# Kernel tuning notes

Measured on AMD Instinct MI355X. Metric: run time of the kernel, lower is better.

The kernel has to match this reference:

```python
import jax, jax.numpy as jnp
import numpy as np

B, S, Q, C = 1, 128, 256, 256
H, DH = 8, 32
TOT = H * DH  # 256


def setup_inputs() -> dict:
    key = jax.random.key(0)
    ks = jax.random.split(key, 12)
    inp = {
        'q_x': jax.random.normal(ks[0], (B, S, Q, C), jnp.float32),
        'kv_x': jax.random.normal(ks[1], (B, S, Q, C), jnp.float32),
        'bias_mask': jax.random.normal(ks[2], (B, S, 1, 1, Q), jnp.float32),
        'bias_pair': jax.random.normal(ks[3], (B, 1, H, Q, Q), jnp.float32),
        # torch nn.Linear weights are (out_features, in_features)
        'Wq': jax.random.normal(ks[4], (TOT, C), jnp.float32) * (C ** -0.5),
        'Wk': jax.random.normal(ks[5], (TOT, C), jnp.float32) * (C ** -0.5),
        'Wv': jax.random.normal(ks[6], (TOT, C), jnp.float32) * (C ** -0.5),
        'Wg': jax.random.normal(ks[7], (TOT, C), jnp.float32) * 0.02,
        'bg': jnp.ones((TOT,), jnp.float32),   # 'gating' init: zero W, bias=1
        'Wo': jax.random.normal(ks[8], (C, TOT), jnp.float32) * 0.02,
        'bo': jnp.zeros((C,), jnp.float32),
    }
    return inp


def reference(q_x, kv_x, bias_mask, bias_pair, Wq, Wk, Wv, Wg, bg, Wo, bo):
    # QKV projections (no bias), split heads, move head dim before Q: [B,S,H,Q,DH]
    def proj(x, W):
        y = jnp.einsum('bsqc,dc->bsqd', x, W)
        return y.reshape(*y.shape[:-1], H, DH).transpose(0, 1, 3, 2, 4)

    q = proj(q_x, Wq)   # NOTE: literal source applies NO 1/sqrt(dh) scaling in naive mode
    k = proj(kv_x, Wk)
    v = proj(kv_x, Wv)

    # scores [B,S,H,Q,K] with additive biases, manual softmax
    scores = jnp.einsum('bshqd,bshkd->bshqk', q, k) + bias_mask + bias_pair
    a = jax.nn.softmax(scores, axis=-1)
    o = jnp.einsum('bshqk,bshkd->bshqd', a, v)
    o = o.transpose(0, 1, 3, 2, 4)  # [B,S,Q,H,DH]

    # gating
    g = jax.nn.sigmoid(jnp.einsum('bsqc,dc->bsqd', q_x, Wg) + bg)
    o = o * g.reshape(*g.shape[:-1], H, DH)

    # output projection
    o = o.reshape(*o.shape[:-2], TOT)
    return jnp.einsum('bsqd,cd->bsqc', o, Wo) + bo
```

## Files before the change

### kernel.cpp

```cpp
#include <hip/hip_runtime.h>


typedef unsigned short u16;
typedef unsigned int   u32;
typedef float  f32x4  __attribute__((ext_vector_type(4)));
typedef __bf16 bf16x8 __attribute__((ext_vector_type(8)));

__device__ __forceinline__ float bf2f(u16 u) {
    union { u32 i; float f; } v; v.i = ((u32)u) << 16; return v.f;
}
__device__ __forceinline__ u16 f2bf(float f) {
    __bf16 h = (__bf16)f; return __builtin_bit_cast(u16, h);
}

__device__ __forceinline__ void gld16(const u16* g, u16* l) {
    __builtin_amdgcn_global_load_lds(
        (const __attribute__((address_space(1))) u32*)g,
        (__attribute__((address_space(3))) u32*)l, 16, 0, 0);
}

__device__ __forceinline__ void cvt8(const float4* src, u16* dst) {
    float4 a = src[0], b = src[1];
    u16 r[8];
    r[0] = f2bf(a.x); r[1] = f2bf(a.y); r[2] = f2bf(a.z); r[3] = f2bf(a.w);
    r[4] = f2bf(b.x); r[5] = f2bf(b.y); r[6] = f2bf(b.z); r[7] = f2bf(b.w);
    *(uint4*)dst = *(uint4*)r;
}

__global__ __launch_bounds__(256) void prep(
    const float* __restrict__ qx, const float* __restrict__ kvx,
    const float* __restrict__ Wq, const float* __restrict__ Wk,
    const float* __restrict__ Wv, const float* __restrict__ Wg,
    const float* __restrict__ Wo,
    u16* __restrict__ Xq, u16* __restrict__ Xkv, u16* __restrict__ Wball)
{
    const int b = blockIdx.x, t = threadIdx.x;
    if (b < 4096) {
        const int e = (b * 256 + t) * 8;
        cvt8((const float4*)(qx + e), Xq + e);
    } else if (b < 8192) {
        const int e = ((b - 4096) * 256 + t) * 8;
        cvt8((const float4*)(kvx + e), Xkv + e);
    } else {
        const int b2  = b - 8192;
        const int mat = b2 >> 5;
        const float* W = (mat == 0) ? Wq : (mat == 1) ? Wk : (mat == 2) ? Wv
                       : (mat == 3) ? Wg : Wo;
        const int off = (b2 & 31) * 2048 + t * 8;
        cvt8((const float4*)(W + off), Wball + mat * 65536 + off);
    }
}

__global__ __launch_bounds__(256) void proj_all(
    const u16* __restrict__ Xq, const u16* __restrict__ Xkv,
    const u16* __restrict__ Wball, const float* __restrict__ bg,
    u16* __restrict__ Qb, u16* __restrict__ Kb, u16* __restrict__ Vb, u16* __restrict__ Gb)
{
    __shared__ u16 At[128 * 64];
    __shared__ u16 Wt[128 * 64];

    const int bid = blockIdx.x;
    const int mb  = bid & 255;
    const int nb  = bid >> 8;
    const int t   = nb >> 1;
    const int n0  = (nb & 1) * 128;
    const int m0  = mb * 128;
    const u16* A = (t == 0 || t == 3) ? Xq : Xkv;
    const u16* W = Wball + t * 65536;
    u16*       O = (t == 0) ? Qb : (t == 1) ? Kb : (t == 2) ? Vb : Gb;

    const int tid  = threadIdx.x;
    const int lane = tid & 63;
    const int w    = tid >> 6;
    const int quad = lane >> 4;
    const int ln   = lane & 15;
    const int wm   = (w >> 1) * 64;
    const int wn   = (w & 1) * 64;
    const int lrow = lane >> 3;
    const int lcol = (lane & 7) * 8;

    f32x4 acc[4][4] = {};

    for (int k0 = 0; k0 < 256; k0 += 64) {
        __syncthreads();
        #pragma unroll
        for (int qq = 0; qq < 4; ++qq) {
            const int r = w * 32 + qq * 8;
            gld16(A + (size_t)(m0 + r + lrow) * 256 + k0 + lcol, &At[r * 64]);
            gld16(W + (size_t)(n0 + r + lrow) * 256 + k0 + lcol, &Wt[r * 64]);
        }
        __syncthreads();

        #pragma unroll
        for (int kk = 0; kk < 2; ++kk) {
            const int kc = kk * 32 + quad * 8;
            bf16x8 af[4], bfr[4];
            #pragma unroll
            for (int i = 0; i < 4; ++i)
                af[i] = __builtin_bit_cast(bf16x8, *(const uint4*)&At[(wm + i * 16 + ln) * 64 + kc]);
            #pragma unroll
            for (int j = 0; j < 4; ++j)
                bfr[j] = __builtin_bit_cast(bf16x8, *(const uint4*)&Wt[(wn + j * 16 + ln) * 64 + kc]);
            #pragma unroll
            for (int i = 0; i < 4; ++i)
                #pragma unroll
                for (int j = 0; j < 4; ++j)
                    acc[i][j] = __builtin_amdgcn_mfma_f32_16x16x32_bf16(af[i], bfr[j], acc[i][j], 0, 0, 0);
        }
    }

    const int act = (t == 3);
    #pragma unroll
    for (int i = 0; i < 4; ++i) {
        #pragma unroll
        for (int j = 0; j < 4; ++j) {
            #pragma unroll
            for (int rr = 0; rr < 4; ++rr) {
                const int row = m0 + wm + i * 16 + quad * 4 + rr;
                const int col = n0 + wn + j * 16 + ln;
                float v = acc[i][j][rr];
                if (act) { v += bg[col]; v = 1.0f / (1.0f + __expf(-v)); }
                O[(size_t)row * 256 + col] = f2bf(v);
            }
        }
    }
}

__global__ __launch_bounds__(256) void gemm_out(
    const u16* __restrict__ Ob, const u16* __restrict__ Wob,
    const float* __restrict__ bo, float* __restrict__ out)
{
    __shared__ u16 At[64 * 64];
    __shared__ u16 Wt[128 * 64];

    const int bid = blockIdx.x;
    const int m0  = (bid & 511) * 64;
    const int n0  = (bid >> 9) * 128;

    const int tid  = threadIdx.x;
    const int lane = tid & 63;
    const int w    = tid >> 6;
    const int quad = lane >> 4;
    const int ln   = lane & 15;
    const int wm   = (w >> 1) * 32;
    const int wn   = (w & 1) * 64;
    const int lrow = lane >> 3;
    const int lcol = (lane & 7) * 8;

    f32x4 acc[2][4] = {};

    for (int k0 = 0; k0 < 256; k0 += 64) {
        __syncthreads();
        #pragma unroll
        for (int qq = 0; qq < 2; ++qq) {
            const int r = w * 16 + qq * 8;
            gld16(Ob + (size_t)(m0 + r + lrow) * 256 + k0 + lcol, &At[r * 64]);
        }
        #pragma unroll
        for (int qq = 0; qq < 4; ++qq) {
            const int r = w * 32 + qq * 8;
            gld16(Wob + (size_t)(n0 + r + lrow) * 256 + k0 + lcol, &Wt[r * 64]);
        }
        __syncthreads();

        #pragma unroll
        for (int kk = 0; kk < 2; ++kk) {
            const int kc = kk * 32 + quad * 8;
            bf16x8 af[2], bfr[4];
            #pragma unroll
            for (int i = 0; i < 2; ++i)
                af[i] = __builtin_bit_cast(bf16x8, *(const uint4*)&At[(wm + i * 16 + ln) * 64 + kc]);
            #pragma unroll
            for (int j = 0; j < 4; ++j)
                bfr[j] = __builtin_bit_cast(bf16x8, *(const uint4*)&Wt[(wn + j * 16 + ln) * 64 + kc]);
            #pragma unroll
            for (int i = 0; i < 2; ++i)
                #pragma unroll
                for (int j = 0; j < 4; ++j)
                    acc[i][j] = __builtin_amdgcn_mfma_f32_16x16x32_bf16(af[i], bfr[j], acc[i][j], 0, 0, 0);
        }
    }

    #pragma unroll
    for (int i = 0; i < 2; ++i) {
        #pragma unroll
        for (int j = 0; j < 4; ++j) {
            #pragma unroll
            for (int rr = 0; rr < 4; ++rr) {
                const int row = m0 + wm + i * 16 + quad * 4 + rr;
                const int col = n0 + wn + j * 16 + ln;
                out[(size_t)row * 256 + col] = acc[i][j][rr] + bo[col];
            }
        }
    }
}

__global__ __launch_bounds__(256) void attn_kernel(
    const u16* __restrict__ Qb, const u16* __restrict__ Kb, const u16* __restrict__ Vb,
    const u16* __restrict__ Gb, const float* __restrict__ bm, const float* __restrict__ bp,
    u16* __restrict__ Ob)
{
    __shared__ u16   Vt[32][264];
    __shared__ u16   Pl[4][16][268];
    __shared__ float bmf[256];

    const int hs   = blockIdx.x;
    const int h    = hs & 7;
    const int s    = hs >> 3;
    const int qt   = blockIdx.y;
    const int tid  = threadIdx.x;
    const int lane = tid & 63;
    const int w    = tid >> 6;
    const int quad = lane >> 4;
    const int ln   = lane & 15;

    {
        const uint4* vp = (const uint4*)(Vb + (size_t)(s * 256 + tid) * 256 + h * 32);
        uint4 vv0 = vp[0], vv1 = vp[1], vv2 = vp[2], vv3 = vp[3];
        u16 tmp[32];
        *(uint4*)&tmp[0]  = vv0; *(uint4*)&tmp[8]  = vv1;
        *(uint4*)&tmp[16] = vv2; *(uint4*)&tmp[24] = vv3;
        #pragma unroll
        for (int dh = 0; dh < 32; ++dh) Vt[dh][tid] = tmp[dh];
        bmf[tid] = bm[s * 256 + tid];
    }
    __syncthreads();

    const int q0 = qt * 64 + w * 16;

    bf16x8 aq = __builtin_bit_cast(bf16x8,
        *(const uint4*)(Qb + (size_t)(s * 256 + q0 + ln) * 256 + h * 32 + quad * 8));

    f32x4 sc[16];
    #pragma unroll
    for (int nt = 0; nt < 16; ++nt) {
        bf16x8 bk = __builtin_bit_cast(bf16x8,
            *(const uint4*)(Kb + (size_t)(s * 256 + nt * 16 + ln) * 256 + h * 32 + quad * 8));
        f32x4 z = {0.f, 0.f, 0.f, 0.f};
        sc[nt] = __builtin_amdgcn_mfma_f32_16x16x32_bf16(aq, bk, z, 0, 0, 0);
    }

    float rmax[4] = {-1e30f, -1e30f, -1e30f, -1e30f};
    #pragma unroll
    for (int nt = 0; nt < 16; ++nt) {
        const int kp = nt * 16 + ln;
        const float bmv = bmf[kp];
        #pragma unroll
        for (int rr = 0; rr < 4; ++rr) {
            const int q = q0 + quad * 4 + rr;
            float v = sc[nt][rr] + bmv + bp[(size_t)(h * 256 + q) * 256 + kp];
            sc[nt][rr] = v;
            rmax[rr] = fmaxf(rmax[rr], v);
        }
    }
    #pragma unroll
    for (int rr = 0; rr < 4; ++rr) {
        float m = rmax[rr];
        m = fmaxf(m, __shfl_xor(m, 1));
        m = fmaxf(m, __shfl_xor(m, 2));
        m = fmaxf(m, __shfl_xor(m, 4));
        m = fmaxf(m, __shfl_xor(m, 8));
        rmax[rr] = m;
    }
    float rsum[4] = {0.f, 0.f, 0.f, 0.f};
    #pragma unroll
    for (int nt = 0; nt < 16; ++nt)
        #pragma unroll
        for (int rr = 0; rr < 4; ++rr) {
            float p = __expf(sc[nt][rr] - rmax[rr]);
            sc[nt][rr] = p;
            rsum[rr] += p;
        }
    float rinv[4];
    #pragma unroll
    for (int rr = 0; rr < 4; ++rr) {
        float t = rsum[rr];
        t += __shfl_xor(t, 1);
        t += __shfl_xor(t, 2);
        t += __shfl_xor(t, 4);
        t += __shfl_xor(t, 8);
        rinv[rr] = 1.0f / t;
    }

    #pragma unroll
    for (int nt = 0; nt < 16; ++nt)
        #pragma unroll
        for (int rr = 0; rr < 4; ++rr)
            Pl[w][quad * 4 + rr][nt * 16 + ln] = f2bf(sc[nt][rr] * rinv[rr]);

    f32x4 o0 = {0.f, 0.f, 0.f, 0.f}, o1 = {0.f, 0.f, 0.f, 0.f};
    #pragma unroll
    for (int kc = 0; kc < 8; ++kc) {
        bf16x8 pa = __builtin_bit_cast(bf16x8, *(const uint4*)&Pl[w][ln][kc * 32 + quad * 8]);
        bf16x8 v0 = __builtin_bit_cast(bf16x8, *(const uint4*)&Vt[ln][kc * 32 + quad * 8]);
        bf16x8 v1 = __builtin_bit_cast(bf16x8, *(const uint4*)&Vt[16 + ln][kc * 32 + quad * 8]);
        o0 = __builtin_amdgcn_mfma_f32_16x16x32_bf16(pa, v0, o0, 0, 0, 0);
        o1 = __builtin_amdgcn_mfma_f32_16x16x32_bf16(pa, v1, o1, 0, 0, 0);
    }

    #pragma unroll
    for (int rr = 0; rr < 4; ++rr) {
        const int q = q0 + quad * 4 + rr;
        const size_t base = (size_t)(s * 256 + q) * 256 + h * 32;
        float g0 = bf2f(Gb[base + ln]);
        float g1 = bf2f(Gb[base + 16 + ln]);
        Ob[base + ln]      = f2bf(o0[rr] * g0);
        Ob[base + 16 + ln] = f2bf(o1[rr] * g1);
    }
}

extern "C" void kernel_launch(void* const* d_in, const int* in_sizes, int n_in,
                              void* d_out, int out_size, void* d_ws, size_t ws_size,
                              hipStream_t stream)
{
    const float* qx  = (const float*)d_in[0];
    const float* kvx = (const float*)d_in[1];
    const float* bm  = (const float*)d_in[2];
    const float* bp  = (const float*)d_in[3];
    const float* Wq  = (const float*)d_in[4];
    const float* Wk  = (const float*)d_in[5];
    const float* Wv  = (const float*)d_in[6];
    const float* Wg  = (const float*)d_in[7];
    const float* bg  = (const float*)d_in[8];
    const float* Wo  = (const float*)d_in[9];
    const float* bo  = (const float*)d_in[10];
    float* out = (float*)d_out;

    const size_t NEL = (size_t)32768 * 256;
    u16* Qb = (u16*)d_ws;
    u16* Kb = Qb + NEL;
    u16* Vb = Kb + NEL;
    u16* Gb = Vb + NEL;
    u16* Wball = Gb + NEL;

    u16* Xq  = (u16*)d_out;
    u16* Xkv = Xq + NEL;

    prep<<<dim3(8352), dim3(256), 0, stream>>>(qx, kvx, Wq, Wk, Wv, Wg, Wo, Xq, Xkv, Wball);

    proj_all<<<dim3(2048), dim3(256), 0, stream>>>(Xq, Xkv, Wball, bg, Qb, Kb, Vb, Gb);

    attn_kernel<<<dim3(1024, 4), dim3(256), 0, stream>>>(Qb, Kb, Vb, Gb, bm, bp, Qb );

    gemm_out<<<dim3(1024), dim3(256), 0, stream>>>(Qb , Wball + 4 * 65536, bo, out);
}
```

Before: 250.1 us.

## Store Q/K/V/G projections in head-major layout for contiguous attention loads

Projection outputs now go to a [H][S][Q][DH] head-major layout instead of row-major [S*Q][256], and the attention and output GEMM kernels index through the new mapping. Each attention block's Q, K, V and G reads become one contiguous 16 KB region per (head, s) rather than 64-byte pieces strided by 512 bytes, which should improve coalescing and cache-line use. The cost is scattered 2-byte stores in the projection epilogue across head slabs, and gemm_out's A-tile loads now gather from four head slabs per 64-column k-chunk.

```diff
diff --git a/kernel.cpp b/kernel.cpp
--- a/kernel.cpp
+++ b/kernel.cpp
@@ -17,6 +17,11 @@
     __builtin_amdgcn_global_load_lds(
         (const __attribute__((address_space(1))) u32*)g,
         (__attribute__((address_space(3))) u32*)l, 16, 0, 0);
+}
+
+__device__ __forceinline__ size_t hm(int row, int col) {
+    const int s = row >> 8, q = row & 255, h = col >> 5, dh = col & 31;
+    return ((size_t)((h * 128 + s) * 256 + q) << 5) + dh;
 }
 
 __device__ __forceinline__ void cvt8(const float4* src, u16* dst) {
@@ -54,7 +59,7 @@
 __global__ __launch_bounds__(256) void proj_all(
     const u16* __restrict__ Xq, const u16* __restrict__ Xkv,
     const u16* __restrict__ Wball, const float* __restrict__ bg,
-    u16* __restrict__ Qb, u16* __restrict__ Kb, u16* __restrict__ Vb, u16* __restrict__ Gb)
+    u16* __restrict__ Qh, u16* __restrict__ Kh, u16* __restrict__ Vh, u16* __restrict__ Gh)
 {
     __shared__ u16 At[128 * 64];
     __shared__ u16 Wt[128 * 64];
@@ -67,7 +72,7 @@
     const int m0  = mb * 128;
     const u16* A = (t == 0 || t == 3) ? Xq : Xkv;
     const u16* W = Wball + t * 65536;
-    u16*       O = (t == 0) ? Qb : (t == 1) ? Kb : (t == 2) ? Vb : Gb;
+    u16*       O = (t == 0) ? Qh : (t == 1) ? Kh : (t == 2) ? Vh : Gh;
 
     const int tid  = threadIdx.x;
     const int lane = tid & 63;
@@ -120,14 +125,14 @@
                 const int col = n0 + wn + j * 16 + ln;
                 float v = acc[i][j][rr];
                 if (act) { v += bg[col]; v = 1.0f / (1.0f + __expf(-v)); }
-                O[(size_t)row * 256 + col] = f2bf(v);
+                O[hm(row, col)] = f2bf(v);
             }
         }
     }
 }
 
 __global__ __launch_bounds__(256) void gemm_out(
-    const u16* __restrict__ Ob, const u16* __restrict__ Wob,
+    const u16* __restrict__ Oh, const u16* __restrict__ Wob,
     const float* __restrict__ bo, float* __restrict__ out)
 {
     __shared__ u16 At[64 * 64];
@@ -154,7 +159,7 @@
         #pragma unroll
         for (int qq = 0; qq < 2; ++qq) {
             const int r = w * 16 + qq * 8;
-            gld16(Ob + (size_t)(m0 + r + lrow) * 256 + k0 + lcol, &At[r * 64]);
+            gld16(Oh + hm(m0 + r + lrow, k0 + lcol), &At[r * 64]);
         }
         #pragma unroll
         for (int qq = 0; qq < 4; ++qq) {
@@ -196,9 +201,9 @@
 }
 
 __global__ __launch_bounds__(256) void attn_kernel(
-    const u16* __restrict__ Qb, const u16* __restrict__ Kb, const u16* __restrict__ Vb,
-    const u16* __restrict__ Gb, const float* __restrict__ bm, const float* __restrict__ bp,
-    u16* __restrict__ Ob)
+    const u16* __restrict__ Qh, const u16* __restrict__ Kh, const u16* __restrict__ Vh,
+    const u16* __restrict__ Gh, const float* __restrict__ bm, const float* __restrict__ bp,
+    u16* __restrict__ Oh)
 {
     __shared__ u16   Vt[32][264];
     __shared__ u16   Pl[4][16][268];
@@ -214,8 +219,10 @@
     const int quad = lane >> 4;
     const int ln   = lane & 15;
 
+    const size_t hsBase = ((size_t)(h * 128 + s) * 256) << 5;
+
     {
-        const uint4* vp = (const uint4*)(Vb + (size_t)(s * 256 + tid) * 256 + h * 32);
+        const uint4* vp = (const uint4*)(Vh + hsBase + (size_t)tid * 32);
         uint4 vv0 = vp[0], vv1 = vp[1], vv2 = vp[2], vv3 = vp[3];
         u16 tmp[32];
         *(uint4*)&tmp[0]  = vv0; *(uint4*)&tmp[8]  = vv1;
@@ -229,13 +236,13 @@
     const int q0 = qt * 64 + w * 16;
 
     bf16x8 aq = __builtin_bit_cast(bf16x8,
-        *(const uint4*)(Qb + (size_t)(s * 256 + q0 + ln) * 256 + h * 32 + quad * 8));
+        *(const uint4*)(Qh + hsBase + (size_t)(q0 + ln) * 32 + quad * 8));
 
     f32x4 sc[16];
     #pragma unroll
     for (int nt = 0; nt < 16; ++nt) {
         bf16x8 bk = __builtin_bit_cast(bf16x8,
-            *(const uint4*)(Kb + (size_t)(s * 256 + nt * 16 + ln) * 256 + h * 32 + quad * 8));
+            *(const uint4*)(Kh + hsBase + (size_t)(nt * 16 + ln) * 32 + quad * 8));
         f32x4 z = {0.f, 0.f, 0.f, 0.f};
         sc[nt] = __builtin_amdgcn_mfma_f32_16x16x32_bf16(aq, bk, z, 0, 0, 0);
     }
@@ -301,11 +308,11 @@
     #pragma unroll
     for (int rr = 0; rr < 4; ++rr) {
         const int q = q0 + quad * 4 + rr;
-        const size_t base = (size_t)(s * 256 + q) * 256 + h * 32;
-        float g0 = bf2f(Gb[base + ln]);
-        float g1 = bf2f(Gb[base + 16 + ln]);
-        Ob[base + ln]      = f2bf(o0[rr] * g0);
-        Ob[base + 16 + ln] = f2bf(o1[rr] * g1);
+        const size_t base = hsBase + (size_t)q * 32;
+        float g0 = bf2f(Gh[base + ln]);
+        float g1 = bf2f(Gh[base + 16 + ln]);
+        Oh[base + ln]      = f2bf(o0[rr] * g0);
+        Oh[base + 16 + ln] = f2bf(o1[rr] * g1);
     }
 }
 
@@ -327,20 +334,20 @@
     float* out = (float*)d_out;
 
     const size_t NEL = (size_t)32768 * 256;
-    u16* Qb = (u16*)d_ws;
-    u16* Kb = Qb + NEL;
-    u16* Vb = Kb + NEL;
-    u16* Gb = Vb + NEL;
-    u16* Wball = Gb + NEL;
+    u16* Qh = (u16*)d_ws;
+    u16* Kh = Qh + NEL;
+    u16* Vh = Kh + NEL;
+    u16* Gh = Vh + NEL;
+    u16* Wball = Gh + NEL;
 
     u16* Xq  = (u16*)d_out;
     u16* Xkv = Xq + NEL;
 
     prep<<<dim3(8352), dim3(256), 0, stream>>>(qx, kvx, Wq, Wk, Wv, Wg, Wo, Xq, Xkv, Wball);
 
-    proj_all<<<dim3(2048), dim3(256), 0, stream>>>(Xq, Xkv, Wball, bg, Qb, Kb, Vb, Gb);
-
-    attn_kernel<<<dim3(1024, 4), dim3(256), 0, stream>>>(Qb, Kb, Vb, Gb, bm, bp, Qb );
-
-    gemm_out<<<dim3(1024), dim3(256), 0, stream>>>(Qb , Wball + 4 * 65536, bo, out);
-}
+    proj_all<<<dim3(2048), dim3(256), 0, stream>>>(Xq, Xkv, Wball, bg, Qh, Kh, Vh, Gh);
+
+    attn_kernel<<<dim3(1024, 4), dim3(256), 0, stream>>>(Qh, Kh, Vh, Gh, bm, bp, Qh );
+
+    gemm_out<<<dim3(1024), dim3(256), 0, stream>>>(Qh , Wball + 4 * 65536, bo, out);
+}
```

Result: faster. 229.9 us (-8.1%).
